# Performance work log

Measured on AMD Instinct MI355X. Metric: run time of the kernel, lower is better.

## Reference

```python
import jax, jax.numpy as jnp
import numpy as np

N, E, G = 20000, 320000, 64
IN_DIM, EDGE_DIM, H, L = 23, 6, 256, 4
NEG = 0.2   # leaky_relu negative slope (GATv2 default)
EPS = 1e-5  # layernorm eps


def setup_inputs() -> dict:
    key = jax.random.key(0)
    ks = jax.random.split(key, 12)
    g = lambda k, shape: jax.random.normal(k, shape, jnp.float32) * 0.05
    return {
        "x": jax.random.normal(ks[0], (N, IN_DIM), jnp.float32),
        "edge_index": jax.random.randint(ks[1], (2, E), 0, N),
        "edge_attr": jax.random.uniform(ks[2], (E, EDGE_DIM), dtype=jnp.float32),
        "batch": jnp.sort(jax.random.randint(ks[3], (N,), 0, G)),
        "W_l0": g(ks[4], (IN_DIM, H)),
        "W_r0": g(ks[5], (IN_DIM, H)),
        "W_l": g(ks[6], (L - 1, H, H)),
        "W_r": g(ks[7], (L - 1, H, H)),
        "b_l": jnp.zeros((L, H), jnp.float32),
        "b_r": jnp.zeros((L, H), jnp.float32),
        "W_e": g(ks[8], (L, EDGE_DIM, H)),
        "att": g(ks[9], (L, H)),
        "bias": jnp.zeros((L, H), jnp.float32),
        "ln_w": jnp.ones((L, H), jnp.float32),
        "ln_b": jnp.zeros((L, H), jnp.float32),
        "lin_W": g(ks[10], (H, H)),
        "lin_b": jnp.zeros((H,), jnp.float32),
    }


def _segment_softmax(logits, seg, n):
    m = jax.ops.segment_max(logits, seg, num_segments=n)  # every node has a self loop -> finite
    e = jnp.exp(logits - m[seg])
    s = jax.ops.segment_sum(e, seg, num_segments=n)
    return e / s[seg]


def _gatv2(h, src, dst, e_emb, Wl, bl, Wr, br, a, bout):
    n = h.shape[0]
    hl = h @ Wl + bl  # source transform [N, H]
    hr = h @ Wr + br  # target transform [N, H]
    m = hl[src] + hr[dst] + e_emb              # [E', H]
    m = jnp.where(m > 0, m, NEG * m)           # leaky_relu
    alpha = _segment_softmax(m @ a, dst, n)    # [E']
    out = jax.ops.segment_sum(hl[src] * alpha[:, None], dst, num_segments=n)
    return out + bout


def _layernorm(x, w, b):
    mu = x.mean(-1, keepdims=True)
    var = ((x - mu) ** 2).mean(-1, keepdims=True)
    return (x - mu) * jax.lax.rsqrt(var + EPS) * w + b


def reference(x, edge_index, edge_attr, batch, W_l0, W_r0, W_l, W_r, b_l, b_r,
              W_e, att, bias, ln_w, ln_b, lin_W, lin_b):
    n = x.shape[0]
    src, dst = edge_index[0], edge_index[1]
    # add self loops; self-loop edge_attr = mean of incoming edge_attr (fill_value='mean')
    ones_e = jnp.ones((src.shape[0],), x.dtype)
    deg = jax.ops.segment_sum(ones_e, dst, num_segments=n)
    loop_attr = jax.ops.segment_sum(edge_attr, dst, num_segments=n) / jnp.maximum(deg, 1.0)[:, None]
    loops = jnp.arange(n, dtype=src.dtype)
    src_f = jnp.concatenate([src, loops])
    dst_f = jnp.concatenate([dst, loops])
    ea = jnp.concatenate([edge_attr, loop_attr], axis=0)  # [E+N, 6]

    Wls = [W_l0] + [W_l[i] for i in range(L - 1)]
    Wrs = [W_r0] + [W_r[i] for i in range(L - 1)]
    h = x
    for i in range(L):
        e_emb = ea @ W_e[i]  # [E+N, H]
        h = _gatv2(h, src_f, dst_f, e_emb, Wls[i], b_l[i], Wrs[i], b_r[i], att[i], bias[i])
        h = _layernorm(h, ln_w[i], ln_b[i])
        h = jax.nn.relu(h)
    h = h @ lin_W + lin_b  # final jk='last' projection
    # global mean pool over graphs
    cnt = jax.ops.segment_sum(jnp.ones((n,), h.dtype), batch, num_segments=G)
    pooled = jax.ops.segment_sum(h, batch, num_segments=G) / jnp.maximum(cnt, 1.0)[:, None]
    return pooled
```

## Files before the change

kernel.cpp:

```cpp
#include <hip/hip_runtime.h>
#include <hip/hip_bf16.h>
#include <math.h>

#define H 256
#define EDIM 6
#define NEG 0.2f
#define LN_EPS 1e-5f
#define NPAD 20096

typedef __bf16 bf16x8 __attribute__((ext_vector_type(8)));
typedef float  floatx4 __attribute__((ext_vector_type(4)));
typedef float  f32x2   __attribute__((ext_vector_type(2)));

__device__ __forceinline__ float b2f(unsigned short u) {
    union { unsigned int i; float f; } v; v.i = ((unsigned int)u) << 16; return v.f;
}
__device__ __forceinline__ unsigned short f2bu(float f) {
    __hip_bfloat16 h = __float2bfloat16(f);
    return *(unsigned short*)&h;
}

__global__ void k_edge_hist(const int* __restrict__ ei, int* __restrict__ deg, int E) {
    int e = blockIdx.x * blockDim.x + threadIdx.x;
    if (e >= E) return;
    atomicAdd(&deg[ei[E + e]], 1);
}

__global__ __launch_bounds__(256) void k_scan1(const int* __restrict__ deg,
                                               int* __restrict__ row_ptr,
                                               int* __restrict__ bsum, int N) {
    __shared__ int ws[4];
    int tid = threadIdx.x, gid = blockIdx.x * 256 + tid;
    int lane = tid & 63, w = tid >> 6;
    int v = (gid < N) ? deg[gid] : 0;
    int x = v;
#pragma unroll
    for (int d = 1; d < 64; d <<= 1) { int y = __shfl_up(x, d); if (lane >= d) x += y; }
    if (lane == 63) ws[w] = x;
    __syncthreads();
    int off = 0;
#pragma unroll
    for (int i = 0; i < 4; i++) off += (i < w) ? ws[i] : 0;
    if (gid < N) row_ptr[gid] = off + x - v;
    if (tid == 255) bsum[blockIdx.x] = off + x;
}

__global__ __launch_bounds__(256) void k_scan2(int* __restrict__ bsum, int nb) {
    __shared__ int ws[4];
    int tid = threadIdx.x;
    int lane = tid & 63, w = tid >> 6;
    int v = (tid < nb) ? bsum[tid] : 0;
    int x = v;
#pragma unroll
    for (int d = 1; d < 64; d <<= 1) { int y = __shfl_up(x, d); if (lane >= d) x += y; }
    if (lane == 63) ws[w] = x;
    __syncthreads();
    int off = 0;
#pragma unroll
    for (int i = 0; i < 4; i++) off += (i < w) ? ws[i] : 0;
    if (tid < nb) bsum[tid] = off + x - v;
}

__global__ __launch_bounds__(256) void k_scan3(int* __restrict__ row_ptr,
                                               int* __restrict__ cursor,
                                               const int* __restrict__ bsum, int N, int E) {
    int gid = blockIdx.x * 256 + threadIdx.x;
    if (gid < N) {
        int v = row_ptr[gid] + bsum[blockIdx.x];
        row_ptr[gid] = v;
        cursor[gid] = v;
    }
    if (gid == 0) row_ptr[N] = E;
}

__global__ void k_scatter(const int* __restrict__ ei, const float* __restrict__ eattr,
                          int* __restrict__ cursor, float4* __restrict__ erec, int E) {
    int e = blockIdx.x * blockDim.x + threadIdx.x;
    if (e >= E) return;
    int s = ei[e], d = ei[E + e];
    int pos = atomicAdd(&cursor[d], 1);
    float4 ra, rb;
    ra.x = __int_as_float(s << 10);
    ra.y = eattr[e * EDIM + 0];
    ra.z = eattr[e * EDIM + 1];
    ra.w = eattr[e * EDIM + 2];
    rb.x = eattr[e * EDIM + 3];
    rb.y = eattr[e * EDIM + 4];
    rb.z = eattr[e * EDIM + 5];
    rb.w = 0.f;
    erec[(size_t)pos * 2]     = ra;
    erec[(size_t)pos * 2 + 1] = rb;
}

__global__ __launch_bounds__(256) void k_loop_mean(const int* __restrict__ row_ptr,
                                                   const float4* __restrict__ erec,
                                                   float* __restrict__ loop_attr, int N) {
    int wv = threadIdx.x >> 6, lane = threadIdx.x & 63;
    int node = blockIdx.x * 4 + wv;
    if (node >= N) return;
    int e0 = row_ptr[node], e1 = row_ptr[node + 1];
    float es[6] = {0.f, 0.f, 0.f, 0.f, 0.f, 0.f};
    for (int e = e0 + lane; e < e1; e += 64) {
        float4 ra = erec[(size_t)e * 2];
        float4 rb = erec[(size_t)e * 2 + 1];
        es[0] += ra.y; es[1] += ra.z; es[2] += ra.w;
        es[3] += rb.x; es[4] += rb.y; es[5] += rb.z;
    }
#pragma unroll
    for (int d = 1; d < 64; d <<= 1) {
#pragma unroll
        for (int k = 0; k < 6; k++) es[k] += __shfl_xor(es[k], d);
    }
    if (lane == 0) {
        float inv = 1.f / fmaxf((float)(e1 - e0), 1.f);
        float4 a, b;
        a.x = es[0] * inv; a.y = es[1] * inv; a.z = es[2] * inv; a.w = es[3] * inv;
        b.x = es[4] * inv; b.y = es[5] * inv; b.z = 0.f; b.w = 0.f;
        *(float4*)&loop_attr[(size_t)node * 8]     = a;
        *(float4*)&loop_attr[(size_t)node * 8 + 4] = b;
    }
}

__global__ void k_conv_x(const float* __restrict__ x, __hip_bfloat16* __restrict__ xb, int N) {
    int idx = blockIdx.x * blockDim.x + threadIdx.x;
    if (idx >= NPAD * 32) return;
    int r = idx >> 5, k = idx & 31;
    float v = (r < N && k < 23) ? x[r * 23 + k] : 0.f;
    xb[idx] = __float2bfloat16(v);
}

__global__ void k_conv_w0(const float* __restrict__ Wl0, const float* __restrict__ Wr0,
                          __hip_bfloat16* __restrict__ out) {
    int idx = blockIdx.x * blockDim.x + threadIdx.x;
    if (idx >= 2 * 256 * 32) return;
    int mat = idx >> 13, rem = idx & 8191;
    int c = rem >> 5, k = rem & 31;
    const float* W = mat ? Wr0 : Wl0;
    float v = (k < 23) ? W[k * 256 + c] : 0.f;
    out[idx] = __float2bfloat16(v);
}

__global__ void k_conv_w(const float* __restrict__ Wl, const float* __restrict__ Wr,
                         __hip_bfloat16* __restrict__ out) {
    int idx = blockIdx.x * blockDim.x + threadIdx.x;
    if (idx >= 6 * 65536) return;
    int mat = idx >> 16, rem = idx & 65535;
    int c = rem >> 8, k = rem & 255;
    const float* W = (mat < 3) ? (Wl + (size_t)mat * 65536)
                   : (Wr + (size_t)(mat - 3) * 65536);
    out[idx] = __float2bfloat16(W[k * 256 + c]);
}

template<int K>
__global__ __launch_bounds__(256) void k_gemm_mfma(
    const __hip_bfloat16* __restrict__ A, int N,
    const __hip_bfloat16* __restrict__ Wt1, const float* __restrict__ b1,
    float* __restrict__ C1,
    const __hip_bfloat16* __restrict__ Wt2, const float* __restrict__ b2,
    float* __restrict__ C2) {
    int tid = threadIdx.x;
    int wv = tid >> 6, lane = tid & 63;
    int quad = lane >> 4, l16 = lane & 15;
    int mat = blockIdx.x >> 1;
    int c0 = (blockIdx.x & 1) * 128;
    int r0 = blockIdx.y * 128;
    const __hip_bfloat16* Wt = mat ? Wt2 : Wt1;
    const float* bv = mat ? b2 : b1;
    float* C = mat ? C2 : C1;
    int wm = wv >> 1, wn = wv & 1;
    int rbase = r0 + wm * 64;
    int cbase = c0 + wn * 64;

    floatx4 acc[4][4] = {};
    const __bf16* Ab = (const __bf16*)A;
    const __bf16* Bb = (const __bf16*)Wt;
#pragma unroll 2
    for (int k0 = 0; k0 < K; k0 += 32) {
        bf16x8 a[4], b[4];
        const __bf16* Ap = Ab + (size_t)(rbase + l16) * K + k0 + quad * 8;
#pragma unroll
        for (int mi = 0; mi < 4; mi++)
            a[mi] = *(const bf16x8*)(Ap + (size_t)mi * 16 * K);
        const __bf16* Bp = Bb + (size_t)(cbase + l16) * K + k0 + quad * 8;
#pragma unroll
        for (int ni = 0; ni < 4; ni++)
            b[ni] = *(const bf16x8*)(Bp + (size_t)ni * 16 * K);
#pragma unroll
        for (int mi = 0; mi < 4; mi++)
#pragma unroll
            for (int ni = 0; ni < 4; ni++)
                acc[mi][ni] = __builtin_amdgcn_mfma_f32_16x16x32_bf16(a[mi], b[ni], acc[mi][ni], 0, 0, 0);
    }
#pragma unroll
    for (int ni = 0; ni < 4; ni++) {
        int c = cbase + ni * 16 + l16;
        float bb = bv[c];
#pragma unroll
        for (int mi = 0; mi < 4; mi++) {
#pragma unroll
            for (int r = 0; r < 4; r++) {
                int gr = rbase + mi * 16 + quad * 4 + r;
                if (gr < N) C[(size_t)gr * H + c] = acc[mi][ni][r] + bb;
            }
        }
    }
}

__global__ __launch_bounds__(256) void k_gat(
    const float* __restrict__ hlf, const float* __restrict__ hr,
    const int* __restrict__ row_ptr, const float4* __restrict__ erec,
    const float* __restrict__ loop_attr,
    const float* __restrict__ We, const float* __restrict__ attv,
    const float* __restrict__ bias, const float* __restrict__ lnw,
    const float* __restrict__ lnb, unsigned short* __restrict__ hout, int N) {
    int wv = threadIdx.x >> 6;
    int lane = threadIdx.x & 63;
    int node = blockIdx.x * 4 + wv;
    if (node >= N) return;
    int cb = lane * 4;
    int cb4 = cb * 4;
    const char* hbase = (const char*)hlf;

    f32x2 we2[EDIM][2];
#pragma unroll
    for (int k = 0; k < EDIM; k++) {
        float4 t = *(const float4*)&We[k * H + cb];
        we2[k][0] = (f32x2){t.x, t.y};
        we2[k][1] = (f32x2){t.z, t.w};
    }
    float4 t;
    t = *(const float4*)&attv[cb];
    f32x2 av0 = {t.x, t.y}, av1 = {t.z, t.w};
    t = *(const float4*)&hr[(size_t)node * H + cb];
    f32x2 hr0 = {t.x, t.y}, hr1 = {t.z, t.w};
    t = *(const float4*)&hlf[(size_t)node * H + cb];
    f32x2 hl0 = {t.x, t.y}, hl1 = {t.z, t.w};

    float denom = 0.f;
    f32x2 acc0 = {0.f, 0.f}, acc1 = {0.f, 0.f};

    int e0 = row_ptr[node], e1 = row_ptr[node + 1];
    int deg = e1 - e0;
    int gfull = deg >> 2;

    for (int g = 0; g < gfull; g++) {
        int base = e0 + g * 4;
        f32x2 hsa[4], hsb[4];
        float p[4];
#pragma unroll
        for (int i = 0; i < 4; i++) {
            float4 ra = erec[(size_t)(base + i) * 2];
            float4 rb = erec[(size_t)(base + i) * 2 + 1];
            float4 h4 = *(const float4*)(hbase + (__float_as_int(ra.x) + cb4));
            hsa[i] = (f32x2){h4.x, h4.y};
            hsb[i] = (f32x2){h4.z, h4.w};
            f32x2 t0 = hr0, t1 = hr1;
            t0 += ra.y * we2[0][0]; t1 += ra.y * we2[0][1];
            t0 += ra.z * we2[1][0]; t1 += ra.z * we2[1][1];
            t0 += ra.w * we2[2][0]; t1 += ra.w * we2[2][1];
            t0 += rb.x * we2[3][0]; t1 += rb.x * we2[3][1];
            t0 += rb.y * we2[4][0]; t1 += rb.y * we2[4][1];
            t0 += rb.z * we2[5][0]; t1 += rb.z * we2[5][1];
            f32x2 v0 = hsa[i] + t0;
            f32x2 v1 = hsb[i] + t1;
            v0 = __builtin_elementwise_max(v0, v0 * NEG);
            v1 = __builtin_elementwise_max(v1, v1 * NEG);
            f32x2 pd = v0 * av0;
            pd += v1 * av1;
            p[i] = pd.x + pd.y;
        }
#pragma unroll
        for (int d = 1; d < 64; d <<= 1) {
#pragma unroll
            for (int i = 0; i < 4; i++) p[i] += __shfl_xor(p[i], d);
        }
        float w0 = __expf(p[0]), w1 = __expf(p[1]);
        float w2 = __expf(p[2]), w3 = __expf(p[3]);
        denom += (w0 + w1) + (w2 + w3);
        acc0 += w0 * hsa[0]; acc1 += w0 * hsb[0];
        acc0 += w1 * hsa[1]; acc1 += w1 * hsb[1];
        acc0 += w2 * hsa[2]; acc1 += w2 * hsb[2];
        acc0 += w3 * hsa[3]; acc1 += w3 * hsb[3];
    }

    int trem = deg & 3;
    if (trem) {
        int base = e0 + gfull * 4;
        f32x2 hsa[4], hsb[4];
        float p[4];
#pragma unroll
        for (int i = 0; i < 4; i++) {
            int idx = (i < trem) ? (base + i) : base;
            float4 ra = erec[(size_t)idx * 2];
            float4 rb = erec[(size_t)idx * 2 + 1];
            float4 h4 = *(const float4*)(hbase + (__float_as_int(ra.x) + cb4));
            hsa[i] = (f32x2){h4.x, h4.y};
            hsb[i] = (f32x2){h4.z, h4.w};
            f32x2 t0 = hr0, t1 = hr1;
            t0 += ra.y * we2[0][0]; t1 += ra.y * we2[0][1];
            t0 += ra.z * we2[1][0]; t1 += ra.z * we2[1][1];
            t0 += ra.w * we2[2][0]; t1 += ra.w * we2[2][1];
            t0 += rb.x * we2[3][0]; t1 += rb.x * we2[3][1];
            t0 += rb.y * we2[4][0]; t1 += rb.y * we2[4][1];
            t0 += rb.z * we2[5][0]; t1 += rb.z * we2[5][1];
            f32x2 v0 = hsa[i] + t0;
            f32x2 v1 = hsb[i] + t1;
            v0 = __builtin_elementwise_max(v0, v0 * NEG);
            v1 = __builtin_elementwise_max(v1, v1 * NEG);
            f32x2 pd = v0 * av0;
            pd += v1 * av1;
            p[i] = pd.x + pd.y;
        }
#pragma unroll
        for (int d = 1; d < 64; d <<= 1) {
#pragma unroll
            for (int i = 0; i < 4; i++) p[i] += __shfl_xor(p[i], d);
        }
        float w[4];
#pragma unroll
        for (int i = 0; i < 4; i++)
            w[i] = (i < trem) ? __expf(p[i]) : 0.f;
        denom += (w[0] + w[1]) + (w[2] + w[3]);
#pragma unroll
        for (int i = 0; i < 4; i++) { acc0 += w[i] * hsa[i]; acc1 += w[i] * hsb[i]; }
    }

    {
        float4 la0 = *(const float4*)&loop_attr[(size_t)node * 8];
        float4 la1 = *(const float4*)&loop_attr[(size_t)node * 8 + 4];
        f32x2 t0 = hl0 + hr0, t1 = hl1 + hr1;
        t0 += la0.x * we2[0][0]; t1 += la0.x * we2[0][1];
        t0 += la0.y * we2[1][0]; t1 += la0.y * we2[1][1];
        t0 += la0.z * we2[2][0]; t1 += la0.z * we2[2][1];
        t0 += la0.w * we2[3][0]; t1 += la0.w * we2[3][1];
        t0 += la1.x * we2[4][0]; t1 += la1.x * we2[4][1];
        t0 += la1.y * we2[5][0]; t1 += la1.y * we2[5][1];
        t0 = __builtin_elementwise_max(t0, t0 * NEG);
        t1 = __builtin_elementwise_max(t1, t1 * NEG);
        f32x2 pd = t0 * av0;
        pd += t1 * av1;
        float p = pd.x + pd.y;
#pragma unroll
        for (int d = 1; d < 64; d <<= 1) p += __shfl_xor(p, d);
        float w = __expf(p);
        denom += w;
        acc0 += w * hl0; acc1 += w * hl1;
    }

    float inv = 1.f / denom;
    t = *(const float4*)&bias[cb];
    float o[4];
    o[0] = acc0.x * inv + t.x;
    o[1] = acc0.y * inv + t.y;
    o[2] = acc1.x * inv + t.z;
    o[3] = acc1.y * inv + t.w;

    float s = o[0] + o[1] + o[2] + o[3];
#pragma unroll
    for (int d = 1; d < 64; d <<= 1) s += __shfl_xor(s, d);
    float mu = s * (1.f / 256.f);
    float vs = 0.f;
#pragma unroll
    for (int j = 0; j < 4; j++) { float dd = o[j] - mu; vs += dd * dd; }
#pragma unroll
    for (int d = 1; d < 64; d <<= 1) vs += __shfl_xor(vs, d);
    float rstd = rsqrtf(vs * (1.f / 256.f) + LN_EPS);

    float4 w4 = *(const float4*)&lnw[cb];
    float4 b4 = *(const float4*)&lnb[cb];
    ushort4 outv;
    outv.x = f2bu(fmaxf((o[0] - mu) * rstd * w4.x + b4.x, 0.f));
    outv.y = f2bu(fmaxf((o[1] - mu) * rstd * w4.y + b4.y, 0.f));
    outv.z = f2bu(fmaxf((o[2] - mu) * rstd * w4.z + b4.z, 0.f));
    outv.w = f2bu(fmaxf((o[3] - mu) * rstd * w4.w + b4.w, 0.f));
    *(ushort4*)&hout[(size_t)node * H + cb] = outv;
}

__global__ __launch_bounds__(256) void k_pool_sum(
    const unsigned short* __restrict__ hb, const int* __restrict__ batch,
    float* __restrict__ pooled, int N) {
    int c = threadIdx.x;
    int chunk = (N + gridDim.x - 1) / gridDim.x;
    int n0 = blockIdx.x * chunk;
    int n1 = min(n0 + chunk, N);
    if (n0 >= n1) return;
    float acc = 0.f;
    int cur = batch[n0];
    for (int n = n0; n < n1; n++) {
        int g = batch[n];
        if (g != cur) {
            atomicAdd(&pooled[cur * H + c], acc);
            acc = 0.f; cur = g;
        }
        acc += b2f(hb[(size_t)n * H + c]);
    }
    atomicAdd(&pooled[cur * H + c], acc);
}

__global__ __launch_bounds__(256) void k_lin_pool(
    const float* __restrict__ pooled, const int* __restrict__ batch,
    const float* __restrict__ linW, const float* __restrict__ linb,
    float* __restrict__ out, int N) {
    __shared__ float row[H];
    __shared__ int s_lo, s_hi;
    int g = blockIdx.x, c = threadIdx.x;
    if (c == 0) {
        int lo = 0, hi = N;
        while (lo < hi) { int mid = (lo + hi) >> 1; if (batch[mid] < g) lo = mid + 1; else hi = mid; }
        s_lo = lo;
    }
    if (c == 1) {
        int lo = 0, hi = N;
        while (lo < hi) { int mid = (lo + hi) >> 1; if (batch[mid] < g + 1) lo = mid + 1; else hi = mid; }
        s_hi = lo;
    }
    __syncthreads();
    int cnt = s_hi - s_lo;
    float scale = (cnt > 0) ? 1.f / (float)cnt : 0.f;
    row[c] = pooled[g * H + c] * scale;
    __syncthreads();
    float acc = (cnt > 0) ? linb[c] : 0.f;
#pragma unroll 8
    for (int k = 0; k < H; k++) acc = fmaf(row[k], linW[k * H + c], acc);
    out[g * H + c] = acc;
}

extern "C" void kernel_launch(void* const* d_in, const int* in_sizes, int n_in,
                              void* d_out, int out_size, void* d_ws, size_t ws_size,
                              hipStream_t stream) {
    const float* x        = (const float*)d_in[0];
    const int*   ei       = (const int*)d_in[1];
    const float* eattr    = (const float*)d_in[2];
    const int*   batch    = (const int*)d_in[3];
    const float* W_l0     = (const float*)d_in[4];
    const float* W_r0     = (const float*)d_in[5];
    const float* W_l      = (const float*)d_in[6];
    const float* W_r      = (const float*)d_in[7];
    const float* b_l      = (const float*)d_in[8];
    const float* b_r      = (const float*)d_in[9];
    const float* W_e      = (const float*)d_in[10];
    const float* att      = (const float*)d_in[11];
    const float* bias     = (const float*)d_in[12];
    const float* ln_w     = (const float*)d_in[13];
    const float* ln_b     = (const float*)d_in[14];
    const float* lin_W    = (const float*)d_in[15];
    const float* lin_b    = (const float*)d_in[16];

    const int N = in_sizes[0] / 23;
    const int E = in_sizes[1] / 2;
    const int G = out_size / H;
    const int L = 4;

    char* p = (char*)d_ws;
    float* hlf = (float*)p;                       p += (size_t)N * H * 4;
    float* hr  = (float*)p;                       p += (size_t)N * H * 4;
    float4* erec = (float4*)p;                    p += (size_t)E * 32;
    unsigned short* hb = (unsigned short*)p;      p += (size_t)NPAD * H * 2;
    __hip_bfloat16* xb  = (__hip_bfloat16*)p;     p += (size_t)NPAD * 32 * 2;
    __hip_bfloat16* w0t = (__hip_bfloat16*)p;     p += (size_t)2 * 256 * 32 * 2;
    __hip_bfloat16* wbig = (__hip_bfloat16*)p;    p += (size_t)6 * 65536 * 2;
    float* loop_attr = (float*)p;                 p += (size_t)N * 8 * 4;
    float* pooled = (float*)p;                    p += (size_t)G * H * 4;
    int* deg      = (int*)p;                      p += (size_t)N * 4;
    int* row_ptr  = (int*)p;                      p += (size_t)(N + 1) * 4;
    int* cursor   = (int*)p;                      p += (size_t)N * 4;
    int* bsum     = (int*)p;                      p += (size_t)256 * 4;

    __hip_bfloat16* Wl0t = w0t;
    __hip_bfloat16* Wr0t = w0t + 8192;
    __hip_bfloat16* Wlt  = wbig;
    __hip_bfloat16* Wrt  = wbig + (size_t)3 * 65536;

    hipMemsetAsync(deg, 0, (size_t)N * sizeof(int), stream);
    hipMemsetAsync(pooled, 0, (size_t)G * H * sizeof(float), stream);
    hipMemsetAsync(hb + (size_t)N * H, 0, (size_t)(NPAD - N) * H * 2, stream);

    int tb = 256;
    k_conv_x<<<(NPAD * 32 + tb - 1) / tb, tb, 0, stream>>>(x, xb, N);
    k_conv_w0<<<(2 * 256 * 32 + tb - 1) / tb, tb, 0, stream>>>(W_l0, W_r0, w0t);
    k_conv_w<<<(6 * 65536 + tb - 1) / tb, tb, 0, stream>>>(W_l, W_r, wbig);

    k_edge_hist<<<(E + tb - 1) / tb, tb, 0, stream>>>(ei, deg, E);
    int nb = (N + 255) / 256;
    k_scan1<<<nb, 256, 0, stream>>>(deg, row_ptr, bsum, N);
    k_scan2<<<1, 256, 0, stream>>>(bsum, nb);
    k_scan3<<<nb, 256, 0, stream>>>(row_ptr, cursor, bsum, N, E);
    k_scatter<<<(E + tb - 1) / tb, tb, 0, stream>>>(ei, eattr, cursor, erec, E);
    k_loop_mean<<<(N + 3) / 4, 256, 0, stream>>>(row_ptr, erec, loop_attr, N);

    dim3 gdual(4, NPAD / 128), blk(256);

    for (int l = 0; l < L; l++) {
        const __hip_bfloat16* A  = (l == 0) ? xb : (const __hip_bfloat16*)hb;
        const __hip_bfloat16* Wl = (l == 0) ? Wl0t : (Wlt + (size_t)(l - 1) * 65536);
        const __hip_bfloat16* Wr = (l == 0) ? Wr0t : (Wrt + (size_t)(l - 1) * 65536);
        if (l == 0)
            k_gemm_mfma<32><<<gdual, blk, 0, stream>>>(A, N, Wl, b_l + l * H, hlf,
                                                       Wr, b_r + l * H, hr);
        else
            k_gemm_mfma<256><<<gdual, blk, 0, stream>>>(A, N, Wl, b_l + l * H, hlf,
                                                        Wr, b_r + l * H, hr);
        k_gat<<<(N + 3) / 4, 256, 0, stream>>>(hlf, hr, row_ptr, erec, loop_attr,
                                               W_e + (size_t)l * EDIM * H, att + l * H,
                                               bias + l * H, ln_w + l * H, ln_b + l * H, hb, N);
    }

    k_pool_sum<<<256, 256, 0, stream>>>(hb, batch, pooled, N);
    k_lin_pool<<<G, 256, 0, stream>>>(pooled, batch, lin_W, lin_b, (float*)d_out, N);
}
```

Baseline: 529.7 us.

## Share A tile across both GEMMs and cut shuffle reductions in GAT kernel

The GEMM now computes both the source and target projections in one block. Each loaded A fragment feeds MFMAs for both weight matrices, with the tile shrunk to 64 rows × 128 columns per matrix. In the GAT kernel, the four per-edge logit reductions are packed into a single butterfly (transpose-style exchange), and the full and tail edge groups are merged into one loop. LayerNorm now does one combined reduction of sum and sum-of-squares instead of two sequential ones. This trades some numerical stability in the variance (E[x²]−μ², clamped at zero) and extra select instructions for fewer shuffles and less A traffic.

```diff
diff --git a/kernel.cpp b/kernel.cpp
--- a/kernel.cpp
+++ b/kernel.cpp
@@ -152,7 +152,7 @@
 }
 
 template<int K>
-__global__ __launch_bounds__(256) void k_gemm_mfma(
+__global__ __launch_bounds__(256) void k_gemm_dual(
     const __hip_bfloat16* __restrict__ A, int N,
     const __hip_bfloat16* __restrict__ Wt1, const float* __restrict__ b1,
     float* __restrict__ C1,
@@ -161,46 +161,52 @@
     int tid = threadIdx.x;
     int wv = tid >> 6, lane = tid & 63;
     int quad = lane >> 4, l16 = lane & 15;
-    int mat = blockIdx.x >> 1;
-    int c0 = (blockIdx.x & 1) * 128;
-    int r0 = blockIdx.y * 128;
-    const __hip_bfloat16* Wt = mat ? Wt2 : Wt1;
-    const float* bv = mat ? b2 : b1;
-    float* C = mat ? C2 : C1;
+    int c0 = blockIdx.x * 128;
+    int r0 = blockIdx.y * 64;
     int wm = wv >> 1, wn = wv & 1;
-    int rbase = r0 + wm * 64;
+    int rbase = r0 + wm * 32;
     int cbase = c0 + wn * 64;
 
-    floatx4 acc[4][4] = {};
+    floatx4 acc1[2][4] = {};
+    floatx4 acc2[2][4] = {};
     const __bf16* Ab = (const __bf16*)A;
-    const __bf16* Bb = (const __bf16*)Wt;
+    const __bf16* B1 = (const __bf16*)Wt1;
+    const __bf16* B2 = (const __bf16*)Wt2;
 #pragma unroll 2
     for (int k0 = 0; k0 < K; k0 += 32) {
-        bf16x8 a[4], b[4];
+        bf16x8 a[2], b1f[4], b2f[4];
         const __bf16* Ap = Ab + (size_t)(rbase + l16) * K + k0 + quad * 8;
 #pragma unroll
-        for (int mi = 0; mi < 4; mi++)
+        for (int mi = 0; mi < 2; mi++)
             a[mi] = *(const bf16x8*)(Ap + (size_t)mi * 16 * K);
-        const __bf16* Bp = Bb + (size_t)(cbase + l16) * K + k0 + quad * 8;
-#pragma unroll
-        for (int ni = 0; ni < 4; ni++)
-            b[ni] = *(const bf16x8*)(Bp + (size_t)ni * 16 * K);
-#pragma unroll
-        for (int mi = 0; mi < 4; mi++)
-#pragma unroll
-            for (int ni = 0; ni < 4; ni++)
-                acc[mi][ni] = __builtin_amdgcn_mfma_f32_16x16x32_bf16(a[mi], b[ni], acc[mi][ni], 0, 0, 0);
+        const __bf16* Bp1 = B1 + (size_t)(cbase + l16) * K + k0 + quad * 8;
+        const __bf16* Bp2 = B2 + (size_t)(cbase + l16) * K + k0 + quad * 8;
+#pragma unroll
+        for (int ni = 0; ni < 4; ni++) {
+            b1f[ni] = *(const bf16x8*)(Bp1 + (size_t)ni * 16 * K);
+            b2f[ni] = *(const bf16x8*)(Bp2 + (size_t)ni * 16 * K);
+        }
+#pragma unroll
+        for (int mi = 0; mi < 2; mi++)
+#pragma unroll
+            for (int ni = 0; ni < 4; ni++) {
+                acc1[mi][ni] = __builtin_amdgcn_mfma_f32_16x16x32_bf16(a[mi], b1f[ni], acc1[mi][ni], 0, 0, 0);
+                acc2[mi][ni] = __builtin_amdgcn_mfma_f32_16x16x32_bf16(a[mi], b2f[ni], acc2[mi][ni], 0, 0, 0);
+            }
     }
 #pragma unroll
     for (int ni = 0; ni < 4; ni++) {
         int c = cbase + ni * 16 + l16;
-        float bb = bv[c];
-#pragma unroll
-        for (int mi = 0; mi < 4; mi++) {
+        float bb1 = b1[c], bb2 = b2[c];
+#pragma unroll
+        for (int mi = 0; mi < 2; mi++) {
 #pragma unroll
             for (int r = 0; r < 4; r++) {
                 int gr = rbase + mi * 16 + quad * 4 + r;
-                if (gr < N) C[(size_t)gr * H + c] = acc[mi][ni][r] + bb;
+                if (gr < N) {
+                    C1[(size_t)gr * H + c] = acc1[mi][ni][r] + bb1;
+                    C2[(size_t)gr * H + c] = acc2[mi][ni][r] + bb2;
+                }
             }
         }
     }
@@ -220,6 +226,8 @@
     int cb = lane * 4;
     int cb4 = cb * 4;
     const char* hbase = (const char*)hlf;
+    bool b0 = (lane & 1) != 0;
+    bool b1 = (lane & 2) != 0;
 
     f32x2 we2[EDIM][2];
 #pragma unroll
@@ -243,49 +251,10 @@
     int deg = e1 - e0;
     int gfull = deg >> 2;
 
-    for (int g = 0; g < gfull; g++) {
+    for (int g = 0; g <= gfull; g++) {
+        int trem = (g == gfull) ? (deg & 3) : 4;
+        if (trem == 0) break;
         int base = e0 + g * 4;
-        f32x2 hsa[4], hsb[4];
-        float p[4];
-#pragma unroll
-        for (int i = 0; i < 4; i++) {
-            float4 ra = erec[(size_t)(base + i) * 2];
-            float4 rb = erec[(size_t)(base + i) * 2 + 1];
-            float4 h4 = *(const float4*)(hbase + (__float_as_int(ra.x) + cb4));
-            hsa[i] = (f32x2){h4.x, h4.y};
-            hsb[i] = (f32x2){h4.z, h4.w};
-            f32x2 t0 = hr0, t1 = hr1;
-            t0 += ra.y * we2[0][0]; t1 += ra.y * we2[0][1];
-            t0 += ra.z * we2[1][0]; t1 += ra.z * we2[1][1];
-            t0 += ra.w * we2[2][0]; t1 += ra.w * we2[2][1];
-            t0 += rb.x * we2[3][0]; t1 += rb.x * we2[3][1];
-            t0 += rb.y * we2[4][0]; t1 += rb.y * we2[4][1];
-            t0 += rb.z * we2[5][0]; t1 += rb.z * we2[5][1];
-            f32x2 v0 = hsa[i] + t0;
-            f32x2 v1 = hsb[i] + t1;
-            v0 = __builtin_elementwise_max(v0, v0 * NEG);
-            v1 = __builtin_elementwise_max(v1, v1 * NEG);
-            f32x2 pd = v0 * av0;
-            pd += v1 * av1;
-            p[i] = pd.x + pd.y;
-        }
-#pragma unroll
-        for (int d = 1; d < 64; d <<= 1) {
-#pragma unroll
-            for (int i = 0; i < 4; i++) p[i] += __shfl_xor(p[i], d);
-        }
-        float w0 = __expf(p[0]), w1 = __expf(p[1]);
-        float w2 = __expf(p[2]), w3 = __expf(p[3]);
-        denom += (w0 + w1) + (w2 + w3);
-        acc0 += w0 * hsa[0]; acc1 += w0 * hsb[0];
-        acc0 += w1 * hsa[1]; acc1 += w1 * hsb[1];
-        acc0 += w2 * hsa[2]; acc1 += w2 * hsb[2];
-        acc0 += w3 * hsa[3]; acc1 += w3 * hsb[3];
-    }
-
-    int trem = deg & 3;
-    if (trem) {
-        int base = e0 + gfull * 4;
         f32x2 hsa[4], hsb[4];
         float p[4];
 #pragma unroll
@@ -311,18 +280,32 @@
             pd += v1 * av1;
             p[i] = pd.x + pd.y;
         }
-#pragma unroll
-        for (int d = 1; d < 64; d <<= 1) {
-#pragma unroll
-            for (int i = 0; i < 4; i++) p[i] += __shfl_xor(p[i], d);
-        }
-        float w[4];
-#pragma unroll
-        for (int i = 0; i < 4; i++)
-            w[i] = (i < trem) ? __expf(p[i]) : 0.f;
-        denom += (w[0] + w[1]) + (w[2] + w[3]);
-#pragma unroll
-        for (int i = 0; i < 4; i++) { acc0 += w[i] * hsa[i]; acc1 += w[i] * hsb[i]; }
+        float a01 = b0 ? p[1] : p[0];
+        float c01 = b0 ? p[0] : p[1];
+        a01 += __shfl_xor(c01, 1);
+        float a23 = b0 ? p[3] : p[2];
+        float c23 = b0 ? p[2] : p[3];
+        a23 += __shfl_xor(c23, 1);
+        float u = b1 ? a23 : a01;
+        float v = b1 ? a01 : a23;
+        u += __shfl_xor(v, 2);
+        u += __shfl_xor(u, 4);
+        u += __shfl_xor(u, 8);
+        u += __shfl_xor(u, 16);
+        u += __shfl_xor(u, 32);
+        float w = ((lane & 3) < trem) ? __expf(u) : 0.f;
+        float wx1 = __shfl_xor(w, 1);
+        float wx2 = __shfl_xor(w, 2);
+        float wx3 = __shfl_xor(wx1, 2);
+        denom += (w + wx1) + (wx2 + wx3);
+        float x0 = b0 ? wx1 : w,   x1 = b0 ? w   : wx1;
+        float x2 = b0 ? wx3 : wx2, x3 = b0 ? wx2 : wx3;
+        float w0 = b1 ? x2 : x0, w1 = b1 ? x3 : x1;
+        float w2 = b1 ? x0 : x2, w3 = b1 ? x1 : x3;
+        acc0 += w0 * hsa[0]; acc1 += w0 * hsb[0];
+        acc0 += w1 * hsa[1]; acc1 += w1 * hsb[1];
+        acc0 += w2 * hsa[2]; acc1 += w2 * hsb[2];
+        acc0 += w3 * hsa[3]; acc1 += w3 * hsb[3];
     }
 
     {
@@ -349,30 +332,35 @@
 
     float inv = 1.f / denom;
     t = *(const float4*)&bias[cb];
-    float o[4];
-    o[0] = acc0.x * inv + t.x;
-    o[1] = acc0.y * inv + t.y;
-    o[2] = acc1.x * inv + t.z;
-    o[3] = acc1.y * inv + t.w;
-
-    float s = o[0] + o[1] + o[2] + o[3];
-#pragma unroll
-    for (int d = 1; d < 64; d <<= 1) s += __shfl_xor(s, d);
-    float mu = s * (1.f / 256.f);
-    float vs = 0.f;
-#pragma unroll
-    for (int j = 0; j < 4; j++) { float dd = o[j] - mu; vs += dd * dd; }
-#pragma unroll
-    for (int d = 1; d < 64; d <<= 1) vs += __shfl_xor(vs, d);
-    float rstd = rsqrtf(vs * (1.f / 256.f) + LN_EPS);
+    float o0 = acc0.x * inv + t.x;
+    float o1 = acc0.y * inv + t.y;
+    float o2 = acc1.x * inv + t.z;
+    float o3 = acc1.y * inv + t.w;
+
+    float s = (o0 + o1) + (o2 + o3);
+    float q = fmaf(o0, o0, fmaf(o1, o1, fmaf(o2, o2, o3 * o3)));
+    float a = b0 ? q : s;
+    float c = b0 ? s : q;
+    a += __shfl_xor(c, 1);
+    a += __shfl_xor(a, 2);
+    a += __shfl_xor(a, 4);
+    a += __shfl_xor(a, 8);
+    a += __shfl_xor(a, 16);
+    a += __shfl_xor(a, 32);
+    float other = __shfl_xor(a, 1);
+    float stot = b0 ? other : a;
+    float qtot = b0 ? a : other;
+    float mu = stot * (1.f / 256.f);
+    float var = fmaf(-mu, mu, qtot * (1.f / 256.f));
+    float rstd = rsqrtf(fmaxf(var, 0.f) + LN_EPS);
 
     float4 w4 = *(const float4*)&lnw[cb];
     float4 b4 = *(const float4*)&lnb[cb];
     ushort4 outv;
-    outv.x = f2bu(fmaxf((o[0] - mu) * rstd * w4.x + b4.x, 0.f));
-    outv.y = f2bu(fmaxf((o[1] - mu) * rstd * w4.y + b4.y, 0.f));
-    outv.z = f2bu(fmaxf((o[2] - mu) * rstd * w4.z + b4.z, 0.f));
-    outv.w = f2bu(fmaxf((o[3] - mu) * rstd * w4.w + b4.w, 0.f));
+    outv.x = f2bu(fmaxf((o0 - mu) * rstd * w4.x + b4.x, 0.f));
+    outv.y = f2bu(fmaxf((o1 - mu) * rstd * w4.y + b4.y, 0.f));
+    outv.z = f2bu(fmaxf((o2 - mu) * rstd * w4.z + b4.z, 0.f));
+    outv.w = f2bu(fmaxf((o3 - mu) * rstd * w4.w + b4.w, 0.f));
     *(ushort4*)&hout[(size_t)node * H + cb] = outv;
 }
 
@@ -488,17 +476,17 @@
     k_scatter<<<(E + tb - 1) / tb, tb, 0, stream>>>(ei, eattr, cursor, erec, E);
     k_loop_mean<<<(N + 3) / 4, 256, 0, stream>>>(row_ptr, erec, loop_attr, N);
 
-    dim3 gdual(4, NPAD / 128), blk(256);
+    dim3 gdual(2, NPAD / 64), blk(256);
 
     for (int l = 0; l < L; l++) {
         const __hip_bfloat16* A  = (l == 0) ? xb : (const __hip_bfloat16*)hb;
         const __hip_bfloat16* Wl = (l == 0) ? Wl0t : (Wlt + (size_t)(l - 1) * 65536);
         const __hip_bfloat16* Wr = (l == 0) ? Wr0t : (Wrt + (size_t)(l - 1) * 65536);
         if (l == 0)
-            k_gemm_mfma<32><<<gdual, blk, 0, stream>>>(A, N, Wl, b_l + l * H, hlf,
+            k_gemm_dual<32><<<gdual, blk, 0, stream>>>(A, N, Wl, b_l + l * H, hlf,
                                                        Wr, b_r + l * H, hr);
         else
-            k_gemm_mfma<256><<<gdual, blk, 0, stream>>>(A, N, Wl, b_l + l * H, hlf,
+            k_gemm_dual<256><<<gdual, blk, 0, stream>>>(A, N, Wl, b_l + l * H, hlf,
                                                         Wr, b_r + l * H, hr);
         k_gat<<<(N + 3) / 4, 256, 0, stream>>>(hlf, hr, row_ptr, erec, loop_attr,
                                                W_e + (size_t)l * EDIM * H, att + l * H,
```

Measured after the change: 547.9 us. +3.4%, slower.

## Process two nodes per wavefront in GAT kernel and merge conversion kernels

Applied to the files above, without the earlier changes.

Each wavefront in the GAT kernel now handles two destination nodes and interleaves their 4-edge groups. The goal is more independent gathers in flight and less per-wave setup, since edge-weight and attention vectors are loaded once for both nodes. The layernorm reduction now computes sum and sum-of-squares in one combined shuffle pass instead of two dependent reductions, trading a slightly less stable variance formula for fewer shuffles. The three fp32→bf16 conversion kernels are fused into one launch. Costs are higher register pressure, half as many waves in flight, and imbalance when the two nodes' degrees differ.

```diff
diff --git a/kernel.cpp b/kernel.cpp
--- a/kernel.cpp
+++ b/kernel.cpp
@@ -121,34 +121,37 @@
     }
 }
 
-__global__ void k_conv_x(const float* __restrict__ x, __hip_bfloat16* __restrict__ xb, int N) {
-    int idx = blockIdx.x * blockDim.x + threadIdx.x;
-    if (idx >= NPAD * 32) return;
-    int r = idx >> 5, k = idx & 31;
-    float v = (r < N && k < 23) ? x[r * 23 + k] : 0.f;
-    xb[idx] = __float2bfloat16(v);
-}
-
-__global__ void k_conv_w0(const float* __restrict__ Wl0, const float* __restrict__ Wr0,
-                          __hip_bfloat16* __restrict__ out) {
-    int idx = blockIdx.x * blockDim.x + threadIdx.x;
-    if (idx >= 2 * 256 * 32) return;
-    int mat = idx >> 13, rem = idx & 8191;
-    int c = rem >> 5, k = rem & 31;
-    const float* W = mat ? Wr0 : Wl0;
-    float v = (k < 23) ? W[k * 256 + c] : 0.f;
-    out[idx] = __float2bfloat16(v);
-}
-
-__global__ void k_conv_w(const float* __restrict__ Wl, const float* __restrict__ Wr,
-                         __hip_bfloat16* __restrict__ out) {
-    int idx = blockIdx.x * blockDim.x + threadIdx.x;
-    if (idx >= 6 * 65536) return;
-    int mat = idx >> 16, rem = idx & 65535;
-    int c = rem >> 8, k = rem & 255;
-    const float* W = (mat < 3) ? (Wl + (size_t)mat * 65536)
-                   : (Wr + (size_t)(mat - 3) * 65536);
-    out[idx] = __float2bfloat16(W[k * 256 + c]);
+__global__ __launch_bounds__(256) void k_conv_all(
+    const float* __restrict__ x, const float* __restrict__ Wl0,
+    const float* __restrict__ Wr0, const float* __restrict__ Wl,
+    const float* __restrict__ Wr,
+    __hip_bfloat16* __restrict__ xb, __hip_bfloat16* __restrict__ w0t,
+    __hip_bfloat16* __restrict__ wbig, int N) {
+    int idx = blockIdx.x * 256 + threadIdx.x;
+    const int XN = NPAD * 32;
+    if (idx < XN) {
+        int r = idx >> 5, k = idx & 31;
+        float v = (r < N && k < 23) ? x[r * 23 + k] : 0.f;
+        xb[idx] = __float2bfloat16(v);
+        return;
+    }
+    idx -= XN;
+    if (idx < 16384) {
+        int mat = idx >> 13, rem = idx & 8191;
+        int c = rem >> 5, k = rem & 31;
+        const float* W = mat ? Wr0 : Wl0;
+        float v = (k < 23) ? W[k * 256 + c] : 0.f;
+        w0t[idx] = __float2bfloat16(v);
+        return;
+    }
+    idx -= 16384;
+    if (idx < 6 * 65536) {
+        int mat = idx >> 16, rem = idx & 65535;
+        int c = rem >> 8, k = rem & 255;
+        const float* W = (mat < 3) ? (Wl + (size_t)mat * 65536)
+                       : (Wr + (size_t)(mat - 3) * 65536);
+        wbig[idx] = __float2bfloat16(W[k * 256 + c]);
+    }
 }
 
 template<int K>
@@ -206,6 +209,155 @@
     }
 }
 
+__device__ __forceinline__ void gat_group4(
+    int base, const char* hbase, const float4* __restrict__ erec,
+    const f32x2 (&we2)[EDIM][2], f32x2 av0, f32x2 av1,
+    f32x2 hrx0, f32x2 hrx1, int cb4,
+    float& denom, f32x2& acc0, f32x2& acc1) {
+    f32x2 hsa[4], hsb[4];
+    float p[4];
+#pragma unroll
+    for (int i = 0; i < 4; i++) {
+        float4 ra = erec[(size_t)(base + i) * 2];
+        float4 rb = erec[(size_t)(base + i) * 2 + 1];
+        float4 h4 = *(const float4*)(hbase + (__float_as_int(ra.x) + cb4));
+        hsa[i] = (f32x2){h4.x, h4.y};
+        hsb[i] = (f32x2){h4.z, h4.w};
+        f32x2 t0 = hrx0, t1 = hrx1;
+        t0 += ra.y * we2[0][0]; t1 += ra.y * we2[0][1];
+        t0 += ra.z * we2[1][0]; t1 += ra.z * we2[1][1];
+        t0 += ra.w * we2[2][0]; t1 += ra.w * we2[2][1];
+        t0 += rb.x * we2[3][0]; t1 += rb.x * we2[3][1];
+        t0 += rb.y * we2[4][0]; t1 += rb.y * we2[4][1];
+        t0 += rb.z * we2[5][0]; t1 += rb.z * we2[5][1];
+        f32x2 v0 = hsa[i] + t0;
+        f32x2 v1 = hsb[i] + t1;
+        v0 = __builtin_elementwise_max(v0, v0 * NEG);
+        v1 = __builtin_elementwise_max(v1, v1 * NEG);
+        f32x2 pd = v0 * av0;
+        pd += v1 * av1;
+        p[i] = pd.x + pd.y;
+    }
+#pragma unroll
+    for (int d = 1; d < 64; d <<= 1) {
+#pragma unroll
+        for (int i = 0; i < 4; i++) p[i] += __shfl_xor(p[i], d);
+    }
+    float w0 = __expf(p[0]), w1 = __expf(p[1]);
+    float w2 = __expf(p[2]), w3 = __expf(p[3]);
+    denom += (w0 + w1) + (w2 + w3);
+    acc0 += w0 * hsa[0]; acc1 += w0 * hsb[0];
+    acc0 += w1 * hsa[1]; acc1 += w1 * hsb[1];
+    acc0 += w2 * hsa[2]; acc1 += w2 * hsb[2];
+    acc0 += w3 * hsa[3]; acc1 += w3 * hsb[3];
+}
+
+__device__ __forceinline__ void gat_group_tail(
+    int base, int trem, const char* hbase, const float4* __restrict__ erec,
+    const f32x2 (&we2)[EDIM][2], f32x2 av0, f32x2 av1,
+    f32x2 hrx0, f32x2 hrx1, int cb4,
+    float& denom, f32x2& acc0, f32x2& acc1) {
+    f32x2 hsa[4], hsb[4];
+    float p[4];
+#pragma unroll
+    for (int i = 0; i < 4; i++) {
+        int idx = (i < trem) ? (base + i) : base;
+        float4 ra = erec[(size_t)idx * 2];
+        float4 rb = erec[(size_t)idx * 2 + 1];
+        float4 h4 = *(const float4*)(hbase + (__float_as_int(ra.x) + cb4));
+        hsa[i] = (f32x2){h4.x, h4.y};
+        hsb[i] = (f32x2){h4.z, h4.w};
+        f32x2 t0 = hrx0, t1 = hrx1;
+        t0 += ra.y * we2[0][0]; t1 += ra.y * we2[0][1];
+        t0 += ra.z * we2[1][0]; t1 += ra.z * we2[1][1];
+        t0 += ra.w * we2[2][0]; t1 += ra.w * we2[2][1];
+        t0 += rb.x * we2[3][0]; t1 += rb.x * we2[3][1];
+        t0 += rb.y * we2[4][0]; t1 += rb.y * we2[4][1];
+        t0 += rb.z * we2[5][0]; t1 += rb.z * we2[5][1];
+        f32x2 v0 = hsa[i] + t0;
+        f32x2 v1 = hsb[i] + t1;
+        v0 = __builtin_elementwise_max(v0, v0 * NEG);
+        v1 = __builtin_elementwise_max(v1, v1 * NEG);
+        f32x2 pd = v0 * av0;
+        pd += v1 * av1;
+        p[i] = pd.x + pd.y;
+    }
+#pragma unroll
+    for (int d = 1; d < 64; d <<= 1) {
+#pragma unroll
+        for (int i = 0; i < 4; i++) p[i] += __shfl_xor(p[i], d);
+    }
+    float w[4];
+#pragma unroll
+    for (int i = 0; i < 4; i++)
+        w[i] = (i < trem) ? __expf(p[i]) : 0.f;
+    denom += (w[0] + w[1]) + (w[2] + w[3]);
+#pragma unroll
+    for (int i = 0; i < 4; i++) { acc0 += w[i] * hsa[i]; acc1 += w[i] * hsb[i]; }
+}
+
+__device__ __forceinline__ void gat_selfloop(
+    int node, const float* __restrict__ loop_attr,
+    const f32x2 (&we2)[EDIM][2], f32x2 av0, f32x2 av1,
+    f32x2 hl0, f32x2 hl1, f32x2 hrx0, f32x2 hrx1,
+    float& denom, f32x2& acc0, f32x2& acc1) {
+    float4 la0 = *(const float4*)&loop_attr[(size_t)node * 8];
+    float4 la1 = *(const float4*)&loop_attr[(size_t)node * 8 + 4];
+    f32x2 t0 = hl0 + hrx0, t1 = hl1 + hrx1;
+    t0 += la0.x * we2[0][0]; t1 += la0.x * we2[0][1];
+    t0 += la0.y * we2[1][0]; t1 += la0.y * we2[1][1];
+    t0 += la0.z * we2[2][0]; t1 += la0.z * we2[2][1];
+    t0 += la0.w * we2[3][0]; t1 += la0.w * we2[3][1];
+    t0 += la1.x * we2[4][0]; t1 += la1.x * we2[4][1];
+    t0 += la1.y * we2[5][0]; t1 += la1.y * we2[5][1];
+    t0 = __builtin_elementwise_max(t0, t0 * NEG);
+    t1 = __builtin_elementwise_max(t1, t1 * NEG);
+    f32x2 pd = t0 * av0;
+    pd += t1 * av1;
+    float p = pd.x + pd.y;
+#pragma unroll
+    for (int d = 1; d < 64; d <<= 1) p += __shfl_xor(p, d);
+    float w = __expf(p);
+    denom += w;
+    acc0 += w * hl0; acc1 += w * hl1;
+}
+
+__device__ __forceinline__ void gat_epilogue(
+    int node, int cb, bool b0, float denom, f32x2 acc0, f32x2 acc1,
+    const float* __restrict__ bias, const float* __restrict__ lnw,
+    const float* __restrict__ lnb, unsigned short* __restrict__ hout) {
+    float inv = 1.f / denom;
+    float4 t = *(const float4*)&bias[cb];
+    float o0 = acc0.x * inv + t.x;
+    float o1 = acc0.y * inv + t.y;
+    float o2 = acc1.x * inv + t.z;
+    float o3 = acc1.y * inv + t.w;
+    float s = (o0 + o1) + (o2 + o3);
+    float q = fmaf(o0, o0, fmaf(o1, o1, fmaf(o2, o2, o3 * o3)));
+    float a = b0 ? q : s;
+    float c = b0 ? s : q;
+    a += __shfl_xor(c, 1);
+    a += __shfl_xor(a, 2);
+    a += __shfl_xor(a, 4);
+    a += __shfl_xor(a, 8);
+    a += __shfl_xor(a, 16);
+    a += __shfl_xor(a, 32);
+    float other = __shfl_xor(a, 1);
+    float stot = b0 ? other : a;
+    float qtot = b0 ? a : other;
+    float mu = stot * (1.f / 256.f);
+    float var = fmaf(-mu, mu, qtot * (1.f / 256.f));
+    float rstd = rsqrtf(fmaxf(var, 0.f) + LN_EPS);
+    float4 w4 = *(const float4*)&lnw[cb];
+    float4 b4 = *(const float4*)&lnb[cb];
+    ushort4 outv;
+    outv.x = f2bu(fmaxf((o0 - mu) * rstd * w4.x + b4.x, 0.f));
+    outv.y = f2bu(fmaxf((o1 - mu) * rstd * w4.y + b4.y, 0.f));
+    outv.z = f2bu(fmaxf((o2 - mu) * rstd * w4.z + b4.z, 0.f));
+    outv.w = f2bu(fmaxf((o3 - mu) * rstd * w4.w + b4.w, 0.f));
+    *(ushort4*)&hout[(size_t)node * H + cb] = outv;
+}
+
 __global__ __launch_bounds__(256) void k_gat(
     const float* __restrict__ hlf, const float* __restrict__ hr,
     const int* __restrict__ row_ptr, const float4* __restrict__ erec,
@@ -215,11 +367,14 @@
     const float* __restrict__ lnb, unsigned short* __restrict__ hout, int N) {
     int wv = threadIdx.x >> 6;
     int lane = threadIdx.x & 63;
-    int node = blockIdx.x * 4 + wv;
-    if (node >= N) return;
+    int nA = blockIdx.x * 8 + wv * 2;
+    if (nA >= N) return;
+    int nB = nA + 1;
+    bool hasB = nB < N;
     int cb = lane * 4;
     int cb4 = cb * 4;
     const char* hbase = (const char*)hlf;
+    bool b0 = (lane & 1) != 0;
 
     f32x2 we2[EDIM][2];
 #pragma unroll
@@ -231,149 +386,62 @@
     float4 t;
     t = *(const float4*)&attv[cb];
     f32x2 av0 = {t.x, t.y}, av1 = {t.z, t.w};
-    t = *(const float4*)&hr[(size_t)node * H + cb];
-    f32x2 hr0 = {t.x, t.y}, hr1 = {t.z, t.w};
-    t = *(const float4*)&hlf[(size_t)node * H + cb];
-    f32x2 hl0 = {t.x, t.y}, hl1 = {t.z, t.w};
-
-    float denom = 0.f;
-    f32x2 acc0 = {0.f, 0.f}, acc1 = {0.f, 0.f};
-
-    int e0 = row_ptr[node], e1 = row_ptr[node + 1];
-    int deg = e1 - e0;
-    int gfull = deg >> 2;
-
-    for (int g = 0; g < gfull; g++) {
-        int base = e0 + g * 4;
-        f32x2 hsa[4], hsb[4];
-        float p[4];
-#pragma unroll
-        for (int i = 0; i < 4; i++) {
-            float4 ra = erec[(size_t)(base + i) * 2];
-            float4 rb = erec[(size_t)(base + i) * 2 + 1];
-            float4 h4 = *(const float4*)(hbase + (__float_as_int(ra.x) + cb4));
-            hsa[i] = (f32x2){h4.x, h4.y};
-            hsb[i] = (f32x2){h4.z, h4.w};
-            f32x2 t0 = hr0, t1 = hr1;
-            t0 += ra.y * we2[0][0]; t1 += ra.y * we2[0][1];
-            t0 += ra.z * we2[1][0]; t1 += ra.z * we2[1][1];
-            t0 += ra.w * we2[2][0]; t1 += ra.w * we2[2][1];
-            t0 += rb.x * we2[3][0]; t1 += rb.x * we2[3][1];
-            t0 += rb.y * we2[4][0]; t1 += rb.y * we2[4][1];
-            t0 += rb.z * we2[5][0]; t1 += rb.z * we2[5][1];
-            f32x2 v0 = hsa[i] + t0;
-            f32x2 v1 = hsb[i] + t1;
-            v0 = __builtin_elementwise_max(v0, v0 * NEG);
-            v1 = __builtin_elementwise_max(v1, v1 * NEG);
-            f32x2 pd = v0 * av0;
-            pd += v1 * av1;
-            p[i] = pd.x + pd.y;
-        }
-#pragma unroll
-        for (int d = 1; d < 64; d <<= 1) {
-#pragma unroll
-            for (int i = 0; i < 4; i++) p[i] += __shfl_xor(p[i], d);
-        }
-        float w0 = __expf(p[0]), w1 = __expf(p[1]);
-        float w2 = __expf(p[2]), w3 = __expf(p[3]);
-        denom += (w0 + w1) + (w2 + w3);
-        acc0 += w0 * hsa[0]; acc1 += w0 * hsb[0];
-        acc0 += w1 * hsa[1]; acc1 += w1 * hsb[1];
-        acc0 += w2 * hsa[2]; acc1 += w2 * hsb[2];
-        acc0 += w3 * hsa[3]; acc1 += w3 * hsb[3];
-    }
-
-    int trem = deg & 3;
-    if (trem) {
-        int base = e0 + gfull * 4;
-        f32x2 hsa[4], hsb[4];
-        float p[4];
-#pragma unroll
-        for (int i = 0; i < 4; i++) {
-            int idx = (i < trem) ? (base + i) : base;
-            float4 ra = erec[(size_t)idx * 2];
-            float4 rb = erec[(size_t)idx * 2 + 1];
-            float4 h4 = *(const float4*)(hbase + (__float_as_int(ra.x) + cb4));
-            hsa[i] = (f32x2){h4.x, h4.y};
-            hsb[i] = (f32x2){h4.z, h4.w};
-            f32x2 t0 = hr0, t1 = hr1;
-            t0 += ra.y * we2[0][0]; t1 += ra.y * we2[0][1];
-            t0 += ra.z * we2[1][0]; t1 += ra.z * we2[1][1];
-            t0 += ra.w * we2[2][0]; t1 += ra.w * we2[2][1];
-            t0 += rb.x * we2[3][0]; t1 += rb.x * we2[3][1];
-            t0 += rb.y * we2[4][0]; t1 += rb.y * we2[4][1];
-            t0 += rb.z * we2[5][0]; t1 += rb.z * we2[5][1];
-            f32x2 v0 = hsa[i] + t0;
-            f32x2 v1 = hsb[i] + t1;
-            v0 = __builtin_elementwise_max(v0, v0 * NEG);
-            v1 = __builtin_elementwise_max(v1, v1 * NEG);
-            f32x2 pd = v0 * av0;
-            pd += v1 * av1;
-            p[i] = pd.x + pd.y;
-        }
-#pragma unroll
-        for (int d = 1; d < 64; d <<= 1) {
-#pragma unroll
-            for (int i = 0; i < 4; i++) p[i] += __shfl_xor(p[i], d);
-        }
-        float w[4];
-#pragma unroll
-        for (int i = 0; i < 4; i++)
-            w[i] = (i < trem) ? __expf(p[i]) : 0.f;
-        denom += (w[0] + w[1]) + (w[2] + w[3]);
-#pragma unroll
-        for (int i = 0; i < 4; i++) { acc0 += w[i] * hsa[i]; acc1 += w[i] * hsb[i]; }
-    }
-
-    {
-        float4 la0 = *(const float4*)&loop_attr[(size_t)node * 8];
-        float4 la1 = *(const float4*)&loop_attr[(size_t)node * 8 + 4];
-        f32x2 t0 = hl0 + hr0, t1 = hl1 + hr1;
-        t0 += la0.x * we2[0][0]; t1 += la0.x * we2[0][1];
-        t0 += la0.y * we2[1][0]; t1 += la0.y * we2[1][1];
-        t0 += la0.z * we2[2][0]; t1 += la0.z * we2[2][1];
-        t0 += la0.w * we2[3][0]; t1 += la0.w * we2[3][1];
-        t0 += la1.x * we2[4][0]; t1 += la1.x * we2[4][1];
-        t0 += la1.y * we2[5][0]; t1 += la1.y * we2[5][1];
-        t0 = __builtin_elementwise_max(t0, t0 * NEG);
-        t1 = __builtin_elementwise_max(t1, t1 * NEG);
-        f32x2 pd = t0 * av0;
-        pd += t1 * av1;
-        float p = pd.x + pd.y;
-#pragma unroll
-        for (int d = 1; d < 64; d <<= 1) p += __shfl_xor(p, d);
-        float w = __expf(p);
-        denom += w;
-        acc0 += w * hl0; acc1 += w * hl1;
-    }
-
-    float inv = 1.f / denom;
-    t = *(const float4*)&bias[cb];
-    float o[4];
-    o[0] = acc0.x * inv + t.x;
-    o[1] = acc0.y * inv + t.y;
-    o[2] = acc1.x * inv + t.z;
-    o[3] = acc1.y * inv + t.w;
-
-    float s = o[0] + o[1] + o[2] + o[3];
-#pragma unroll
-    for (int d = 1; d < 64; d <<= 1) s += __shfl_xor(s, d);
-    float mu = s * (1.f / 256.f);
-    float vs = 0.f;
-#pragma unroll
-    for (int j = 0; j < 4; j++) { float dd = o[j] - mu; vs += dd * dd; }
-#pragma unroll
-    for (int d = 1; d < 64; d <<= 1) vs += __shfl_xor(vs, d);
-    float rstd = rsqrtf(vs * (1.f / 256.f) + LN_EPS);
-
-    float4 w4 = *(const float4*)&lnw[cb];
-    float4 b4 = *(const float4*)&lnb[cb];
-    ushort4 outv;
-    outv.x = f2bu(fmaxf((o[0] - mu) * rstd * w4.x + b4.x, 0.f));
-    outv.y = f2bu(fmaxf((o[1] - mu) * rstd * w4.y + b4.y, 0.f));
-    outv.z = f2bu(fmaxf((o[2] - mu) * rstd * w4.z + b4.z, 0.f));
-    outv.w = f2bu(fmaxf((o[3] - mu) * rstd * w4.w + b4.w, 0.f));
-    *(ushort4*)&hout[(size_t)node * H + cb] = outv;
+
+    t = *(const float4*)&hr[(size_t)nA * H + cb];
+    f32x2 hrA0 = {t.x, t.y}, hrA1 = {t.z, t.w};
+    t = *(const float4*)&hlf[(size_t)nA * H + cb];
+    f32x2 hlA0 = {t.x, t.y}, hlA1 = {t.z, t.w};
+    int e0A = row_ptr[nA], e1A = row_ptr[nA + 1];
+
+    f32x2 hrB0 = {0.f, 0.f}, hrB1 = {0.f, 0.f};
+    f32x2 hlB0 = {0.f, 0.f}, hlB1 = {0.f, 0.f};
+    int e0B = 0, e1B = 0;
+    if (hasB) {
+        t = *(const float4*)&hr[(size_t)nB * H + cb];
+        hrB0 = (f32x2){t.x, t.y}; hrB1 = (f32x2){t.z, t.w};
+        t = *(const float4*)&hlf[(size_t)nB * H + cb];
+        hlB0 = (f32x2){t.x, t.y}; hlB1 = (f32x2){t.z, t.w};
+        e0B = row_ptr[nB]; e1B = row_ptr[nB + 1];
+    }
+
+    int degA = e1A - e0A, degB = e1B - e0B;
+    int fgA = degA >> 2, tailA = degA & 3;
+    int fgB = degB >> 2, tailB = degB & 3;
+
+    float denA = 0.f, denB = 0.f;
+    f32x2 accA0 = {0.f, 0.f}, accA1 = {0.f, 0.f};
+    f32x2 accB0 = {0.f, 0.f}, accB1 = {0.f, 0.f};
+
+    int common = min(fgA, fgB);
+    int gA = 0, gB = 0;
+    for (; gA < common; gA++, gB++) {
+        gat_group4(e0A + gA * 4, hbase, erec, we2, av0, av1, hrA0, hrA1, cb4,
+                   denA, accA0, accA1);
+        gat_group4(e0B + gB * 4, hbase, erec, we2, av0, av1, hrB0, hrB1, cb4,
+                   denB, accB0, accB1);
+    }
+    for (; gA < fgA; gA++)
+        gat_group4(e0A + gA * 4, hbase, erec, we2, av0, av1, hrA0, hrA1, cb4,
+                   denA, accA0, accA1);
+    for (; gB < fgB; gB++)
+        gat_group4(e0B + gB * 4, hbase, erec, we2, av0, av1, hrB0, hrB1, cb4,
+                   denB, accB0, accB1);
+    if (tailA)
+        gat_group_tail(e0A + fgA * 4, tailA, hbase, erec, we2, av0, av1,
+                       hrA0, hrA1, cb4, denA, accA0, accA1);
+    if (tailB)
+        gat_group_tail(e0B + fgB * 4, tailB, hbase, erec, we2, av0, av1,
+                       hrB0, hrB1, cb4, denB, accB0, accB1);
+
+    gat_selfloop(nA, loop_attr, we2, av0, av1, hlA0, hlA1, hrA0, hrA1,
+                 denA, accA0, accA1);
+    if (hasB)
+        gat_selfloop(nB, loop_attr, we2, av0, av1, hlB0, hlB1, hrB0, hrB1,
+                     denB, accB0, accB1);
+
+    gat_epilogue(nA, cb, b0, denA, accA0, accA1, bias, lnw, lnb, hout);
+    if (hasB)
+        gat_epilogue(nB, cb, b0, denB, accB0, accB1, bias, lnw, lnb, hout);
 }
 
 __global__ __launch_bounds__(256) void k_pool_sum(
@@ -476,9 +544,9 @@
     hipMemsetAsync(hb + (size_t)N * H, 0, (size_t)(NPAD - N) * H * 2, stream);
 
     int tb = 256;
-    k_conv_x<<<(NPAD * 32 + tb - 1) / tb, tb, 0, stream>>>(x, xb, N);
-    k_conv_w0<<<(2 * 256 * 32 + tb - 1) / tb, tb, 0, stream>>>(W_l0, W_r0, w0t);
-    k_conv_w<<<(6 * 65536 + tb - 1) / tb, tb, 0, stream>>>(W_l, W_r, wbig);
+    int conv_total = NPAD * 32 + 16384 + 6 * 65536;
+    k_conv_all<<<(conv_total + tb - 1) / tb, tb, 0, stream>>>(x, W_l0, W_r0, W_l, W_r,
+                                                              xb, w0t, wbig, N);
 
     k_edge_hist<<<(E + tb - 1) / tb, tb, 0, stream>>>(ei, deg, E);
     int nb = (N + 255) / 256;
@@ -500,7 +568,7 @@
         else
             k_gemm_mfma<256><<<gdual, blk, 0, stream>>>(A, N, Wl, b_l + l * H, hlf,
                                                         Wr, b_r + l * H, hr);
-        k_gat<<<(N + 3) / 4, 256, 0, stream>>>(hlf, hr, row_ptr, erec, loop_attr,
+        k_gat<<<(N + 7) / 8, 256, 0, stream>>>(hlf, hr, row_ptr, erec, loop_attr,
                                                W_e + (size_t)l * EDIM * H, att + l * H,
                                                bias + l * H, ln_w + l * H, ln_b + l * H, hb, N);
     }
```

Measured after the change: 845.5 us. 59.6% more time.
